# Kernel optimization log

Measured on AMD Instinct MI355X. Metric: run time of the kernel, lower is better.

## Reference

```python
import jax, jax.numpy as jnp
import numpy as np

NUM_HEADS = 16


def setup_inputs() -> dict:
    key = jax.random.key(0)
    ks = jax.random.split(key, 5)
    B, S, D = 2, 2048, 2048
    scale = 1.0 / np.sqrt(D)
    return {
        "x": jax.random.normal(ks[0], (B, S, D), dtype=jnp.float32),
        "W_q": jax.random.normal(ks[1], (D, D), dtype=jnp.float32) * scale,
        "W_k": jax.random.normal(ks[2], (D, D), dtype=jnp.float32) * scale,
        "W_v": jax.random.normal(ks[3], (D, D), dtype=jnp.float32) * scale,
        "W_o": jax.random.normal(ks[4], (D, D), dtype=jnp.float32) * scale,
        "b_o": jnp.zeros((D,), dtype=jnp.float32),
    }


def reference(x, W_q, W_k, W_v, W_o, b_o):
    B, S, D = x.shape
    H = NUM_HEADS
    hd = D // H
    # projections, split into heads: [B, H, S, hd]
    q = (x @ W_q).reshape(B, S, H, hd).transpose(0, 2, 1, 3)
    k = (x @ W_k).reshape(B, S, H, hd).transpose(0, 2, 1, 3)
    v = (x @ W_v).reshape(B, S, H, hd).transpose(0, 2, 1, 3)
    # causal attention with explicit score matrix [B, H, S, S]
    scores = jnp.einsum("bhqd,bhkd->bhqk", q, k) / jnp.sqrt(jnp.asarray(hd, x.dtype))
    causal = jnp.tril(jnp.ones((S, S), dtype=bool))  # True = keep
    scores = jnp.where(causal, scores, -jnp.inf)
    weights = jax.nn.softmax(scores, axis=-1)
    ctx = jnp.einsum("bhqk,bhkd->bhqd", weights, v)
    ctx = ctx.transpose(0, 2, 1, 3).reshape(B, S, D)
    return ctx @ W_o + b_o
```

## Files before the change

kernel.cpp:

```cpp
#include <hip/hip_runtime.h>
#include <stdint.h>

#define SQ_S 2048
#define DIM 2048
#define NH 16
#define HD 128
#define NB 2
#define NROWS (NB * SQ_S)
#define NQK (2 * DIM)

typedef __bf16 bf16x8 __attribute__((ext_vector_type(8)));
typedef float f32x4 __attribute__((ext_vector_type(4)));
typedef unsigned short u16;

__device__ __forceinline__ u16 f2bf(float f) {
    unsigned int u = __float_as_uint(f);
    u += 0x7FFF + ((u >> 16) & 1);
    return (u16)(u >> 16);
}

__device__ __forceinline__ void load_lds16(const u16* g, u16* lds) {
    __builtin_amdgcn_global_load_lds(
        (const __attribute__((address_space(1))) unsigned int*)(uintptr_t)g,
        (__attribute__((address_space(3))) unsigned int*)(unsigned int)(uintptr_t)lds,
        16, 0, 0);
}

__global__ __launch_bounds__(256) void cast_x_kernel(const float* __restrict__ in,
                                                     u16* __restrict__ out) {
    int i = (blockIdx.x * 256 + threadIdx.x) * 4;
    float4 v = *(const float4*)(in + i);
    ushort4 o;
    o.x = f2bf(v.x); o.y = f2bf(v.y); o.z = f2bf(v.z); o.w = f2bf(v.w);
    *(ushort4*)(out + i) = o;
}

__global__ __launch_bounds__(256) void transpose_w_kernel(
    const float* __restrict__ w0, const float* __restrict__ w1,
    const float* __restrict__ w2, const float* __restrict__ w3,
    u16* __restrict__ o0, u16* __restrict__ o1,
    u16* __restrict__ o2, u16* __restrict__ o3) {
    __shared__ u16 tile[64][65];
    int z = blockIdx.z;
    const float* in = z == 0 ? w0 : z == 1 ? w1 : z == 2 ? w2 : w3;
    u16* out = z == 0 ? o0 : z == 1 ? o1 : z == 2 ? o2 : o3;
    int r0 = blockIdx.y * 64, c0 = blockIdx.x * 64;
    int t = threadIdx.x;
#pragma unroll
    for (int i = 0; i < 16; ++i) {
        int idx = i * 256 + t;
        int r = idx >> 6, c = idx & 63;
        tile[r][c] = f2bf(in[(size_t)(r0 + r) * DIM + c0 + c]);
    }
    __syncthreads();
#pragma unroll
    for (int i = 0; i < 4; ++i) {
        int idx = i * 256 + t;
        int oc = idx >> 4;
        int r4 = (idx & 15) * 4;
        ushort4 v;
        v.x = tile[r4 + 0][oc]; v.y = tile[r4 + 1][oc];
        v.z = tile[r4 + 2][oc]; v.w = tile[r4 + 3][oc];
        *(ushort4*)(out + (size_t)(c0 + oc) * DIM + r0 + r4) = v;
    }
}

__global__ __launch_bounds__(256) void gemm_bt_bf16(const u16* __restrict__ A,
                                                    const u16* __restrict__ Bt,
                                                    u16* __restrict__ C,
                                                    int M, int N, int K) {
    __shared__ u16 As[128 * 64];
    __shared__ u16 Bs[128 * 64];
    int t = threadIdx.x;
    int w = t >> 6, l = t & 63;
    int wm = (w >> 1) * 64, wn = (w & 1) * 64;
    int lr = l & 15, q = l >> 4;
    int bm = blockIdx.y, bn = blockIdx.x;
    int st_gcol = (((t & 7) ^ ((t >> 3) & 7)) * 8);
    f32x4 acc[4][4] = {};

    for (int k0 = 0; k0 < K; k0 += 64) {
        __syncthreads();
#pragma unroll
        for (int c = 0; c < 4; ++c) {
            int e = c * 2048 + t * 8;
            int row = e >> 6;
            load_lds16(A + (size_t)(bm * 128 + row) * K + k0 + st_gcol, As + e);
        }
#pragma unroll
        for (int c = 0; c < 4; ++c) {
            int e = c * 2048 + t * 8;
            int row = e >> 6;
            load_lds16(Bt + (size_t)(bn * 128 + row) * K + k0 + st_gcol, Bs + e);
        }
        __syncthreads();
#pragma unroll
        for (int kk = 0; kk < 2; ++kk) {
            bf16x8 a[4], b[4];
#pragma unroll
            for (int mt = 0; mt < 4; ++mt)
                a[mt] = *(const bf16x8*)(As + (wm + mt * 16 + lr) * 64 +
                                         (((kk * 4 + q) ^ (lr & 7)) * 8));
#pragma unroll
            for (int nt = 0; nt < 4; ++nt)
                b[nt] = *(const bf16x8*)(Bs + (wn + nt * 16 + lr) * 64 +
                                         (((kk * 4 + q) ^ (lr & 7)) * 8));
#pragma unroll
            for (int mt = 0; mt < 4; ++mt)
#pragma unroll
                for (int nt = 0; nt < 4; ++nt)
                    acc[mt][nt] = __builtin_amdgcn_mfma_f32_16x16x32_bf16(a[mt], b[nt], acc[mt][nt], 0, 0, 0);
        }
    }
    int r0 = bm * 128 + wm, c0 = bn * 128 + wn;
#pragma unroll
    for (int mt = 0; mt < 4; ++mt)
#pragma unroll
        for (int nt = 0; nt < 4; ++nt)
#pragma unroll
            for (int r = 0; r < 4; ++r) {
                int row = r0 + mt * 16 + q * 4 + r;
                int col = c0 + nt * 16 + lr;
                C[(size_t)row * N + col] = f2bf(acc[mt][nt][r]);
            }
}

__global__ __launch_bounds__(256) void gemm_bt_f32b(const u16* __restrict__ A,
                                                    const u16* __restrict__ Bt,
                                                    float* __restrict__ C,
                                                    const float* __restrict__ bias,
                                                    int M, int N, int K) {
    __shared__ u16 As[128 * 64];
    __shared__ u16 Bs[128 * 64];
    int t = threadIdx.x;
    int w = t >> 6, l = t & 63;
    int wm = (w >> 1) * 64, wn = (w & 1) * 64;
    int lr = l & 15, q = l >> 4;
    int bm = blockIdx.y, bn = blockIdx.x;
    int st_gcol = (((t & 7) ^ ((t >> 3) & 7)) * 8);
    f32x4 acc[4][4] = {};

    for (int k0 = 0; k0 < K; k0 += 64) {
        __syncthreads();
#pragma unroll
        for (int c = 0; c < 4; ++c) {
            int e = c * 2048 + t * 8;
            int row = e >> 6;
            load_lds16(A + (size_t)(bm * 128 + row) * K + k0 + st_gcol, As + e);
        }
#pragma unroll
        for (int c = 0; c < 4; ++c) {
            int e = c * 2048 + t * 8;
            int row = e >> 6;
            load_lds16(Bt + (size_t)(bn * 128 + row) * K + k0 + st_gcol, Bs + e);
        }
        __syncthreads();
#pragma unroll
        for (int kk = 0; kk < 2; ++kk) {
            bf16x8 a[4], b[4];
#pragma unroll
            for (int mt = 0; mt < 4; ++mt)
                a[mt] = *(const bf16x8*)(As + (wm + mt * 16 + lr) * 64 +
                                         (((kk * 4 + q) ^ (lr & 7)) * 8));
#pragma unroll
            for (int nt = 0; nt < 4; ++nt)
                b[nt] = *(const bf16x8*)(Bs + (wn + nt * 16 + lr) * 64 +
                                         (((kk * 4 + q) ^ (lr & 7)) * 8));
#pragma unroll
            for (int mt = 0; mt < 4; ++mt)
#pragma unroll
                for (int nt = 0; nt < 4; ++nt)
                    acc[mt][nt] = __builtin_amdgcn_mfma_f32_16x16x32_bf16(a[mt], b[nt], acc[mt][nt], 0, 0, 0);
        }
    }
    int r0 = bm * 128 + wm, c0 = bn * 128 + wn;
#pragma unroll
    for (int mt = 0; mt < 4; ++mt)
#pragma unroll
        for (int nt = 0; nt < 4; ++nt)
#pragma unroll
            for (int r = 0; r < 4; ++r) {
                int row = r0 + mt * 16 + q * 4 + r;
                int col = c0 + nt * 16 + lr;
                C[(size_t)row * N + col] = acc[mt][nt][r] + bias[col];
            }
}

__global__ __launch_bounds__(256) void attn_kernel(const u16* __restrict__ Q,
                                                   const u16* __restrict__ K,
                                                   const u16* __restrict__ Vt,
                                                   u16* __restrict__ ctx,
                                                   int ldqk, int ldv) {
    __shared__ u16 Kl[2][64 * 128];
    __shared__ u16 Vl[2][128 * 64];
    __shared__ u16 Pl[4][16 * 64];
    int t = threadIdx.x;
    int w = t >> 6, l = t & 63;
    int lr = l & 15, q = l >> 4, lk = q * 8;
    int px = blockIdx.x, h = blockIdx.y, b = blockIdx.z;
    const float scale = 0.08838834764831845f;
    int stK_gcol = (((t & 15) ^ (t >> 4)) * 8);
    int stV_gcol = (((t & 7) ^ ((t >> 3) & 7)) * 8);
    const u16* Kbase = K + (size_t)b * SQ_S * ldqk + h * HD;
    const u16* Vbase = Vt + (size_t)(h * HD) * ldv + b * SQ_S;

#pragma unroll 1
    for (int pass = 0; pass < 2; ++pass) {
        int qt = pass == 0 ? px : 31 - px;
        int q0 = qt * 64;
        int njt = qt + 1;

        bf16x8 qf[4];
        {
            const u16* qp = Q + ((size_t)(b * SQ_S + q0 + w * 16 + lr)) * ldqk + h * HD;
#pragma unroll
            for (int kd = 0; kd < 4; ++kd)
                qf[kd] = *(const bf16x8*)(qp + kd * 32 + lk);
        }

        f32x4 o[8] = {};
        float l_r[4] = {0.f, 0.f, 0.f, 0.f};

        {
            int e = t * 8;
#pragma unroll
            for (int c = 0; c < 4; ++c) {
                int eK = c * 2048 + e;
                load_lds16(Kbase + (size_t)(eK >> 7) * ldqk + stK_gcol, Kl[0] + eK);
            }
#pragma unroll
            for (int c = 0; c < 4; ++c) {
                int eV = c * 2048 + e;
                load_lds16(Vbase + (size_t)(eV >> 6) * ldv + stV_gcol, Vl[0] + eV);
            }
        }

#pragma unroll 1
        for (int jt = 0; jt < njt; ++jt) {
            __syncthreads();
            if (jt + 1 < njt) {
                int j1 = (jt + 1) * 64;
                u16* Kd = Kl[(jt + 1) & 1];
                u16* Vd = Vl[(jt + 1) & 1];
                int e = t * 8;
#pragma unroll
                for (int c = 0; c < 4; ++c) {
                    int eK = c * 2048 + e;
                    load_lds16(Kbase + (size_t)(j1 + (eK >> 7)) * ldqk + stK_gcol, Kd + eK);
                }
#pragma unroll
                for (int c = 0; c < 4; ++c) {
                    int eV = c * 2048 + e;
                    load_lds16(Vbase + (size_t)(eV >> 6) * ldv + j1 + stV_gcol, Vd + eV);
                }
            }
            const u16* Kc = Kl[jt & 1];
            const u16* Vc = Vl[jt & 1];

            f32x4 s[4] = {};
#pragma unroll
            for (int kd = 0; kd < 4; ++kd) {
#pragma unroll
                for (int nt = 0; nt < 4; ++nt) {
                    bf16x8 kb = *(const bf16x8*)(Kc + (nt * 16 + lr) * 128 +
                                                 (((kd * 4 + q) ^ lr) * 8));
                    s[nt] = __builtin_amdgcn_mfma_f32_16x16x32_bf16(qf[kd], kb, s[nt], 0, 0, 0);
                }
            }
            bool diag = (jt == qt);
            float rs[4] = {0.f, 0.f, 0.f, 0.f};
            float pv[4][4];
#pragma unroll
            for (int nt = 0; nt < 4; ++nt)
#pragma unroll
                for (int r = 0; r < 4; ++r) {
                    float v = s[nt][r] * scale - 6.0f;
                    if (diag && (nt * 16 + lr > w * 16 + q * 4 + r)) v = -1.0e30f;
                    float pp = __expf(v);
                    pv[nt][r] = pp;
                    rs[r] += pp;
                }
#pragma unroll
            for (int d = 1; d < 16; d <<= 1)
#pragma unroll
                for (int r = 0; r < 4; ++r)
                    rs[r] += __shfl_xor(rs[r], d, 64);
#pragma unroll
            for (int r = 0; r < 4; ++r)
                l_r[r] += rs[r];
            u16* pw = Pl[w];
#pragma unroll
            for (int nt = 0; nt < 4; ++nt)
#pragma unroll
                for (int r = 0; r < 4; ++r) {
                    int prow = q * 4 + r;
                    int pcol = nt * 16 + lr;
                    pw[prow * 64 + (((pcol >> 3) ^ (prow & 7)) * 8) + (pcol & 7)] = f2bf(pv[nt][r]);
                }
            asm volatile("s_waitcnt lgkmcnt(0)" ::: "memory");
#pragma unroll
            for (int kj = 0; kj < 2; ++kj) {
                bf16x8 pa = *(const bf16x8*)(pw + lr * 64 + (((kj * 4 + q) ^ (lr & 7)) * 8));
#pragma unroll
                for (int nd = 0; nd < 8; ++nd) {
                    bf16x8 vb = *(const bf16x8*)(Vc + (nd * 16 + lr) * 64 +
                                                 (((kj * 4 + q) ^ (lr & 7)) * 8));
                    o[nd] = __builtin_amdgcn_mfma_f32_16x16x32_bf16(pa, vb, o[nd], 0, 0, 0);
                }
            }
        }
        float li[4];
#pragma unroll
        for (int r = 0; r < 4; ++r) li[r] = 1.f / l_r[r];
#pragma unroll
        for (int nd = 0; nd < 8; ++nd)
#pragma unroll
            for (int r = 0; r < 4; ++r) {
                int row = q0 + w * 16 + q * 4 + r;
                int col = h * HD + nd * 16 + lr;
                ctx[((size_t)(b * SQ_S + row)) * DIM + col] = f2bf(o[nd][r] * li[r]);
            }
        __syncthreads();
    }
}

extern "C" void kernel_launch(void* const* d_in, const int* in_sizes, int n_in,
                              void* d_out, int out_size, void* d_ws, size_t ws_size,
                              hipStream_t stream) {
    const float* x  = (const float*)d_in[0];
    const float* Wq = (const float*)d_in[1];
    const float* Wk = (const float*)d_in[2];
    const float* Wv = (const float*)d_in[3];
    const float* Wo = (const float*)d_in[4];
    const float* bo = (const float*)d_in[5];
    float* out = (float*)d_out;

    char* p = (char*)d_ws;
    const size_t SZ_ACT = (size_t)NROWS * DIM * 2;
    const size_t SZ_W   = (size_t)DIM * DIM * 2;
    u16* Xb   = (u16*)(p);
    u16* Wqkt = (u16*)(p + SZ_ACT);
    u16* Wvt  = (u16*)(p + SZ_ACT + 2 * SZ_W);
    u16* Wot  = (u16*)(p + SZ_ACT + 3 * SZ_W);
    u16* QK   = (u16*)(p + SZ_ACT + 4 * SZ_W);
    u16* Vt   = (u16*)(p + 3 * SZ_ACT + 4 * SZ_W);
    u16* Cx   = (u16*)(p + 4 * SZ_ACT + 4 * SZ_W);

    cast_x_kernel<<<(NROWS * DIM) / 1024, 256, 0, stream>>>(x, Xb);
    transpose_w_kernel<<<dim3(DIM / 64, DIM / 64, 4), 256, 0, stream>>>(
        Wq, Wk, Wv, Wo,
        Wqkt, Wqkt + (size_t)DIM * DIM, Wvt, Wot);
    gemm_bt_bf16<<<dim3(NQK / 128, NROWS / 128), 256, 0, stream>>>(Xb, Wqkt, QK, NROWS, NQK, DIM);
    gemm_bt_bf16<<<dim3(NROWS / 128, DIM / 128), 256, 0, stream>>>(Wvt, Xb, Vt, DIM, NROWS, DIM);
    attn_kernel<<<dim3(16, NH, NB), 256, 0, stream>>>(QK, QK + DIM, Vt, Cx, NQK, NROWS);
    gemm_bt_f32b<<<dim3(DIM / 128, NROWS / 128), 256, 0, stream>>>(Cx, Wot, out, bo, NROWS, DIM, DIM);
}
```

Measured before the change: 410.1 us.

## Fuse QKV projections into one GEMM and add separate V transpose

```diff
diff --git a/kernel.cpp b/kernel.cpp
--- a/kernel.cpp
+++ b/kernel.cpp
@@ -7,7 +7,7 @@
 #define HD 128
 #define NB 2
 #define NROWS (NB * SQ_S)
-#define NQK (2 * DIM)
+#define NQKV (3 * DIM)
 
 typedef __bf16 bf16x8 __attribute__((ext_vector_type(8)));
 typedef float f32x4 __attribute__((ext_vector_type(4)));
@@ -65,6 +65,28 @@
     }
 }
 
+__global__ __launch_bounds__(256) void transpose_v_kernel(const u16* __restrict__ V,
+                                                          u16* __restrict__ Vt, int ldv) {
+    __shared__ u16 tile[64][72];
+    int s0 = blockIdx.x * 64, d0 = blockIdx.y * 64;
+    int bh = blockIdx.z;
+    int b = bh >> 4, h = bh & 15;
+    int t = threadIdx.x;
+#pragma unroll
+    for (int i = 0; i < 16; ++i) {
+        int idx = i * 256 + t;
+        int r = idx >> 6, c = idx & 63;
+        tile[r][c] = V[((size_t)(b * SQ_S + s0 + r)) * ldv + h * HD + d0 + c];
+    }
+    __syncthreads();
+#pragma unroll
+    for (int i = 0; i < 16; ++i) {
+        int idx = i * 256 + t;
+        int r = idx >> 6, c = idx & 63;
+        Vt[((size_t)(bh * HD + d0 + r)) * SQ_S + s0 + c] = tile[c][r];
+    }
+}
+
 __global__ __launch_bounds__(256) void gemm_bt_bf16(const u16* __restrict__ A,
                                                     const u16* __restrict__ Bt,
                                                     u16* __restrict__ C,
@@ -189,20 +211,23 @@
 __global__ __launch_bounds__(256) void attn_kernel(const u16* __restrict__ Q,
                                                    const u16* __restrict__ K,
                                                    const u16* __restrict__ Vt,
-                                                   u16* __restrict__ ctx,
-                                                   int ldqk, int ldv) {
+                                                   u16* __restrict__ ctx, int ldqk) {
     __shared__ u16 Kl[2][64 * 128];
     __shared__ u16 Vl[2][128 * 64];
     __shared__ u16 Pl[4][16 * 64];
     int t = threadIdx.x;
     int w = t >> 6, l = t & 63;
     int lr = l & 15, q = l >> 4, lk = q * 8;
-    int px = blockIdx.x, h = blockIdx.y, b = blockIdx.z;
+    int bid = blockIdx.x;
+    int r_  = bid >> 3;
+    int px  = r_ & 15;
+    int h   = (bid & 7) + ((r_ >> 4) & 1) * 8;
+    int b   = r_ >> 5;
     const float scale = 0.08838834764831845f;
     int stK_gcol = (((t & 15) ^ (t >> 4)) * 8);
     int stV_gcol = (((t & 7) ^ ((t >> 3) & 7)) * 8);
     const u16* Kbase = K + (size_t)b * SQ_S * ldqk + h * HD;
-    const u16* Vbase = Vt + (size_t)(h * HD) * ldv + b * SQ_S;
+    const u16* Vbase = Vt + ((size_t)(b * NH + h)) * HD * SQ_S;
 
 #pragma unroll 1
     for (int pass = 0; pass < 2; ++pass) {
@@ -231,7 +256,7 @@
 #pragma unroll
             for (int c = 0; c < 4; ++c) {
                 int eV = c * 2048 + e;
-                load_lds16(Vbase + (size_t)(eV >> 6) * ldv + stV_gcol, Vl[0] + eV);
+                load_lds16(Vbase + (size_t)(eV >> 6) * SQ_S + stV_gcol, Vl[0] + eV);
             }
         }
 
@@ -251,7 +276,7 @@
 #pragma unroll
                 for (int c = 0; c < 4; ++c) {
                     int eV = c * 2048 + e;
-                    load_lds16(Vbase + (size_t)(eV >> 6) * ldv + j1 + stV_gcol, Vd + eV);
+                    load_lds16(Vbase + (size_t)(eV >> 6) * SQ_S + j1 + stV_gcol, Vd + eV);
                 }
             }
             const u16* Kc = Kl[jt & 1];
@@ -336,22 +361,22 @@
     float* out = (float*)d_out;
 
     char* p = (char*)d_ws;
-    const size_t SZ_ACT = (size_t)NROWS * DIM * 2;
-    const size_t SZ_W   = (size_t)DIM * DIM * 2;
+    const size_t SZ_ACT  = (size_t)NROWS * DIM * 2;
+    const size_t SZ_W    = (size_t)DIM * DIM * 2;
+    const size_t SZ_QKV  = (size_t)NROWS * NQKV * 2;
     u16* Xb   = (u16*)(p);
-    u16* Wqkt = (u16*)(p + SZ_ACT);
-    u16* Wvt  = (u16*)(p + SZ_ACT + 2 * SZ_W);
+    u16* Wqkv = (u16*)(p + SZ_ACT);
     u16* Wot  = (u16*)(p + SZ_ACT + 3 * SZ_W);
-    u16* QK   = (u16*)(p + SZ_ACT + 4 * SZ_W);
-    u16* Vt   = (u16*)(p + 3 * SZ_ACT + 4 * SZ_W);
-    u16* Cx   = (u16*)(p + 4 * SZ_ACT + 4 * SZ_W);
+    u16* QKV  = (u16*)(p + SZ_ACT + 4 * SZ_W);
+    u16* Vt   = (u16*)(p + SZ_ACT + 4 * SZ_W + SZ_QKV);
+    u16* Cx   = (u16*)(p + 2 * SZ_ACT + 4 * SZ_W + SZ_QKV);
 
     cast_x_kernel<<<(NROWS * DIM) / 1024, 256, 0, stream>>>(x, Xb);
     transpose_w_kernel<<<dim3(DIM / 64, DIM / 64, 4), 256, 0, stream>>>(
         Wq, Wk, Wv, Wo,
-        Wqkt, Wqkt + (size_t)DIM * DIM, Wvt, Wot);
-    gemm_bt_bf16<<<dim3(NQK / 128, NROWS / 128), 256, 0, stream>>>(Xb, Wqkt, QK, NROWS, NQK, DIM);
-    gemm_bt_bf16<<<dim3(NROWS / 128, DIM / 128), 256, 0, stream>>>(Wvt, Xb, Vt, DIM, NROWS, DIM);
-    attn_kernel<<<dim3(16, NH, NB), 256, 0, stream>>>(QK, QK + DIM, Vt, Cx, NQK, NROWS);
+        Wqkv, Wqkv + (size_t)DIM * DIM, Wqkv + 2 * (size_t)DIM * DIM, Wot);
+    gemm_bt_bf16<<<dim3(NQKV / 128, NROWS / 128), 256, 0, stream>>>(Xb, Wqkv, QKV, NROWS, NQKV, DIM);
+    transpose_v_kernel<<<dim3(SQ_S / 64, HD / 64, NB * NH), 256, 0, stream>>>(QKV + 2 * DIM, Vt, NQKV);
+    attn_kernel<<<512, 256, 0, stream>>>(QKV, QKV + DIM, Vt, Cx, NQKV);
     gemm_bt_f32b<<<dim3(DIM / 128, NROWS / 128), 256, 0, stream>>>(Cx, Wot, out, bo, NROWS, DIM, DIM);
 }
```

New measurement: 382.2 us. 6.8% less time.
